# Optimization experiments

Measured on AMD Instinct MI355X. Metric: run time of the kernel, lower is better.

## Reference

```python
import jax, jax.numpy as jnp
import numpy as np

DVEC = 128
B, S = 4, 1024


def setup_inputs() -> dict:
    key = jax.random.key(0)
    k1, k2 = jax.random.split(key)
    func_and_arg = jax.random.normal(k1, (B, S, 2 * DVEC), dtype=jnp.float32)
    cooccurrences = jax.random.normal(k2, (DVEC, DVEC, DVEC), dtype=jnp.float32)
    return {"func_and_arg": func_and_arg, "cooccurrences": cooccurrences}


def reference(func_and_arg, cooccurrences):
    # out[b,s,z] = sum_{i,j} func[b,s,i] * cooc[i,j,z] * arg[b,s,j]
    d = cooccurrences.shape[0]
    func = func_and_arg[..., :d]   # [B,S,D]
    arg = func_and_arg[..., d:]    # [B,S,D]
    # contract func over i first -> [B,S,D(j),Z], then arg over j -> [B,S,Z]
    tmp = jnp.einsum('bsi,ijz->bsjz', func, cooccurrences)
    return jnp.einsum('bsjz,bsj->bsz', tmp, arg)
```

## Files before the change

### kernel.cpp

```cpp
#include <hip/hip_runtime.h>
#include <hip/hip_bf16.h>


typedef __attribute__((ext_vector_type(8))) short bf16x8;
typedef __attribute__((ext_vector_type(4))) float f32x4;

__device__ __forceinline__ unsigned pkbf16(float x, float y) {
    __hip_bfloat162 h = __float22bfloat162_rn(make_float2(x, y));
    unsigned u; __builtin_memcpy(&u, &h, sizeof(u));
    return u;
}

template<int USE_WS>
__global__ __launch_bounds__(256, 2) void cooc_main(
    const float* __restrict__ fa, const float* __restrict__ Cc,
    float* __restrict__ dst)
{
    __shared__ __align__(16) ushort bT[2][64 * 136];
    __shared__ float f_lds[16][128];

    const int bid   = blockIdx.x;
    const int kp    = bid & 7;
    const int zp    = (bid >> 3) & 1;
    const int mtile = bid >> 4;
    const int t0 = mtile * 128;
    const int i0 = kp * 16;
    const int z0 = zp * 64;

    const int tid  = threadIdx.x;
    const int lane = tid & 63;
    const int wv = tid >> 6;
    const int mg = wv >> 1;
    const int zg = wv & 1;
    const int lm = lane & 15;
    const int lk = lane >> 4;

    {
        const int row = tid & 127;
        const int sh = (tid >> 7) * 8;
        const float* fp = fa + (size_t)(t0 + row) * 256 + i0 + sh;
        float4 v0 = *(const float4*)fp;
        float4 v1 = *(const float4*)(fp + 4);
        f_lds[sh + 0][row] = v0.x; f_lds[sh + 1][row] = v0.y;
        f_lds[sh + 2][row] = v0.z; f_lds[sh + 3][row] = v0.w;
        f_lds[sh + 4][row] = v1.x; f_lds[sh + 5][row] = v1.y;
        f_lds[sh + 6][row] = v1.z; f_lds[sh + 7][row] = v1.w;
    }

    union { unsigned u[4]; bf16x8 v; } a_pk[4][4];
    #pragma unroll
    for (int m = 0; m < 4; ++m) {
        const float* ab = fa + (size_t)(t0 + mg * 64 + m * 16 + lm) * 256 + 128;
        #pragma unroll
        for (int ks = 0; ks < 4; ++ks) {
            float4 q0 = *(const float4*)(ab + ks * 32 + lk * 8);
            float4 q1 = *(const float4*)(ab + ks * 32 + lk * 8 + 4);
            a_pk[m][ks].u[0] = pkbf16(q0.x, q0.y);
            a_pk[m][ks].u[1] = pkbf16(q0.z, q0.w);
            a_pk[m][ks].u[2] = pkbf16(q1.x, q1.y);
            a_pk[m][ks].u[3] = pkbf16(q1.z, q1.w);
        }
    }

    const int zq  = tid & 15;
    const int jq0 = tid >> 4;
    const float* csrc0 = Cc + (size_t)i0 * 16384 + (size_t)(jq0 * 4) * 128 + z0 + zq * 4;
    const float* csrc1 = csrc0 + 16 * 4 * 128;
    union { float4 v4[4]; float f[16]; } La[2];

    auto loads = [&](int s) {
        const float* p0 = csrc0 + (size_t)s * 16384;
        const float* p1 = csrc1 + (size_t)s * 16384;
        #pragma unroll
        for (int r = 0; r < 4; ++r) {
            La[0].v4[r] = *(const float4*)(p0 + r * 128);
            La[1].v4[r] = *(const float4*)(p1 + r * 128);
        }
    };
    auto writes = [&](int b) {
        #pragma unroll
        for (int part = 0; part < 2; ++part) {
            const int jq = jq0 + part * 16;
            const int pos = ((jq >> 1) + zq) & 15;
            #pragma unroll
            for (int rr = 0; rr < 4; ++rr) {
                const int zl = zq * 4 + rr;
                const unsigned lo = pkbf16(La[part].f[0 * 4 + rr], La[part].f[1 * 4 + rr]);
                const unsigned hi = pkbf16(La[part].f[2 * 4 + rr], La[part].f[3 * 4 + rr]);
                *(uint2*)&bT[b][zl * 136 + pos * 8 + (jq & 1) * 4] = make_uint2(lo, hi);
            }
        }
    };

    loads(0); writes(0);
    __syncthreads();

    float acc[4][2][4];
    #pragma unroll
    for (int m = 0; m < 4; ++m)
        #pragma unroll
        for (int n = 0; n < 2; ++n)
            #pragma unroll
            for (int r = 0; r < 4; ++r) acc[m][n][r] = 0.f;

    #pragma unroll 2
    for (int s = 0; s < 16; ++s) {
        const int p = s & 1;
        if (s < 15) loads(s + 1);

        float4 f4[4];
        #pragma unroll
        for (int m = 0; m < 4; ++m)
            f4[m] = *(const float4*)&f_lds[s][mg * 64 + m * 16 + lk * 4];

        bf16x8 Bf[4][2];
        #pragma unroll
        for (int ks = 0; ks < 4; ++ks)
            #pragma unroll
            for (int n = 0; n < 2; ++n) {
                const int zz = zg * 32 + n * 16 + lm;
                const int pos = ((ks * 4 + lk) + (zz >> 2)) & 15;
                Bf[ks][n] = *(const bf16x8*)&bT[p][zz * 136 + pos * 8];
            }

        #pragma unroll
        for (int m = 0; m < 4; ++m)
            #pragma unroll
            for (int n = 0; n < 2; ++n) {
                f32x4 g = {0.f, 0.f, 0.f, 0.f};
                #pragma unroll
                for (int ks = 0; ks < 4; ++ks)
                    g = __builtin_amdgcn_mfma_f32_16x16x32_bf16(a_pk[m][ks].v, Bf[ks][n], g, 0, 0, 0);
                acc[m][n][0] += f4[m].x * g[0];
                acc[m][n][1] += f4[m].y * g[1];
                acc[m][n][2] += f4[m].z * g[2];
                acc[m][n][3] += f4[m].w * g[3];
            }

        if (s < 15) writes(p ^ 1);
        __syncthreads();
    }

    #pragma unroll
    for (int m = 0; m < 4; ++m)
        #pragma unroll
        for (int n = 0; n < 2; ++n)
            #pragma unroll
            for (int r = 0; r < 4; ++r) {
                const int row = t0 + mg * 64 + m * 16 + lk * 4 + r;
                const int col = z0 + zg * 32 + n * 16 + lm;
                if (USE_WS)
                    dst[(size_t)kp * 524288 + (size_t)row * 128 + col] = acc[m][n][r];
                else
                    atomicAdd(&dst[(size_t)row * 128 + col], acc[m][n][r]);
            }
}

__global__ __launch_bounds__(256) void cooc_reduce(const float* __restrict__ ws,
                                                   float* __restrict__ out) {
    const size_t idx = ((size_t)blockIdx.x * 256 + threadIdx.x) * 4;
    float4 a = *(const float4*)(ws + idx);
    #pragma unroll
    for (int k = 1; k < 8; ++k) {
        float4 b = *(const float4*)(ws + (size_t)k * 524288 + idx);
        a.x += b.x; a.y += b.y; a.z += b.z; a.w += b.w;
    }
    *(float4*)(out + idx) = a;
}

extern "C" void kernel_launch(void* const* d_in, const int* in_sizes, int n_in,
                              void* d_out, int out_size, void* d_ws, size_t ws_size,
                              hipStream_t stream) {
    const float* fa = (const float*)d_in[0];
    const float* Cc = (const float*)d_in[1];
    float* out = (float*)d_out;

    const bool use_ws = ws_size >= (size_t)8 * 524288 * sizeof(float);
    if (use_ws) {
        cooc_main<1><<<512, 256, 0, stream>>>(fa, Cc, (float*)d_ws);
        cooc_reduce<<<512, 256, 0, stream>>>((const float*)d_ws, out);
    } else {
        (void)hipMemsetAsync(out, 0, (size_t)out_size * sizeof(float), stream);
        cooc_main<0><<<512, 256, 0, stream>>>(fa, Cc, out);
    }
}
```

Baseline: 92.06 us.

## Pre-transpose cooccurrence tensor to bf16 and load MFMA B operands from global

Adds a pre-pass kernel that converts the cooccurrence tensor to bf16 in a z-major transposed layout in workspace. The main kernel then reads B fragments straight from global memory into registers, double-buffered, with no LDS staging or per-step barriers. Each wave now covers all 128 rows for a 16-column slice, holding 8 A tiles in registers. This removes the per-block fp32 conversion, the LDS transpose and the synchronisation, in exchange for an extra launch, extra workspace traffic and higher register pressure. The old path is kept as a fallback for small workspaces.

Result: slower. 104.5 us (+13.6%).

```diff
diff --git a/kernel.cpp b/kernel.cpp
--- a/kernel.cpp
+++ b/kernel.cpp
@@ -11,29 +11,48 @@
     return u;
 }
 
+__global__ __launch_bounds__(256) void cooc_transpose(
+    const float* __restrict__ Cc, ushort* __restrict__ CT)
+{
+    __shared__ float tile[32][132];
+    const int i  = blockIdx.x >> 2;
+    const int j0 = (blockIdx.x & 3) * 32;
+    const int t  = threadIdx.x;
+
+    {
+        const int jj = t >> 3;
+        const int zb = (t & 7) * 16;
+        const float* src = Cc + (size_t)i * 16384 + (size_t)(j0 + jj) * 128 + zb;
+        #pragma unroll
+        for (int k = 0; k < 4; ++k)
+            *(float4*)&tile[jj][zb + k * 4] = *(const float4*)(src + k * 4);
+    }
+    __syncthreads();
+    {
+        const int z = t >> 1;
+        const int h = t & 1;
+        unsigned o[8];
+        #pragma unroll
+        for (int p = 0; p < 8; ++p)
+            o[p] = pkbf16(tile[h * 16 + 2 * p][z], tile[h * 16 + 2 * p + 1][z]);
+        ushort* dst = CT + (size_t)i * 16384 + (size_t)z * 128 + j0 + h * 16;
+        *(uint4*)dst       = make_uint4(o[0], o[1], o[2], o[3]);
+        *(uint4*)(dst + 8) = make_uint4(o[4], o[5], o[6], o[7]);
+    }
+}
+
 template<int USE_WS>
 __global__ __launch_bounds__(256, 2) void cooc_main(
-    const float* __restrict__ fa, const float* __restrict__ Cc,
+    const float* __restrict__ fa, const ushort* __restrict__ CT,
     float* __restrict__ dst)
 {
-    __shared__ __align__(16) ushort bT[2][64 * 136];
     __shared__ float f_lds[16][128];
 
-    const int bid   = blockIdx.x;
-    const int kp    = bid & 7;
-    const int zp    = (bid >> 3) & 1;
-    const int mtile = bid >> 4;
-    const int t0 = mtile * 128;
-    const int i0 = kp * 16;
-    const int z0 = zp * 64;
-
-    const int tid  = threadIdx.x;
-    const int lane = tid & 63;
-    const int wv = tid >> 6;
-    const int mg = wv >> 1;
-    const int zg = wv & 1;
-    const int lm = lane & 15;
-    const int lk = lane >> 4;
+    const int bid = blockIdx.x;
+    const int kp = bid & 7, zp = (bid >> 3) & 1, mtile = bid >> 4;
+    const int t0 = mtile * 128, i0 = kp * 16, z0 = zp * 64;
+    const int tid = threadIdx.x, lane = tid & 63, wv = tid >> 6;
+    const int lm = lane & 15, lk = lane >> 4;
 
     {
         const int row = tid & 127;
@@ -47,10 +66,10 @@
         f_lds[sh + 6][row] = v1.z; f_lds[sh + 7][row] = v1.w;
     }
 
-    union { unsigned u[4]; bf16x8 v; } a_pk[4][4];
-    #pragma unroll
-    for (int m = 0; m < 4; ++m) {
-        const float* ab = fa + (size_t)(t0 + mg * 64 + m * 16 + lm) * 256 + 128;
+    union { unsigned u[4]; bf16x8 v; } a_pk[8][4];
+    #pragma unroll
+    for (int m = 0; m < 8; ++m) {
+        const float* ab = fa + (size_t)(t0 + m * 16 + lm) * 256 + 128;
         #pragma unroll
         for (int ks = 0; ks < 4; ++ks) {
             float4 q0 = *(const float4*)(ab + ks * 32 + lk * 8);
@@ -61,13 +80,110 @@
             a_pk[m][ks].u[3] = pkbf16(q1.z, q1.w);
         }
     }
-
-    const int zq  = tid & 15;
-    const int jq0 = tid >> 4;
+    __syncthreads();
+
+    const ushort* bsrc = CT + (size_t)i0 * 16384
+                            + (size_t)(z0 + wv * 16 + lm) * 128 + lk * 8;
+
+    bf16x8 B[2][4];
+    #pragma unroll
+    for (int ks = 0; ks < 4; ++ks)
+        B[0][ks] = *(const bf16x8*)(bsrc + ks * 32);
+
+    float acc[8][4];
+    #pragma unroll
+    for (int m = 0; m < 8; ++m)
+        #pragma unroll
+        for (int r = 0; r < 4; ++r) acc[m][r] = 0.f;
+
+    #pragma unroll 2
+    for (int s = 0; s < 16; ++s) {
+        const int cur = s & 1;
+        if (s < 15) {
+            const ushort* p = bsrc + (size_t)(s + 1) * 16384;
+            #pragma unroll
+            for (int ks = 0; ks < 4; ++ks)
+                B[cur ^ 1][ks] = *(const bf16x8*)(p + ks * 32);
+        }
+        #pragma unroll
+        for (int m = 0; m < 8; ++m) {
+            float4 f4 = *(const float4*)&f_lds[s][m * 16 + lk * 4];
+            f32x4 g = {0.f, 0.f, 0.f, 0.f};
+            #pragma unroll
+            for (int ks = 0; ks < 4; ++ks)
+                g = __builtin_amdgcn_mfma_f32_16x16x32_bf16(a_pk[m][ks].v, B[cur][ks], g, 0, 0, 0);
+            acc[m][0] += f4.x * g[0];
+            acc[m][1] += f4.y * g[1];
+            acc[m][2] += f4.z * g[2];
+            acc[m][3] += f4.w * g[3];
+        }
+    }
+
+    const int col = z0 + wv * 16 + lm;
+    #pragma unroll
+    for (int m = 0; m < 8; ++m)
+        #pragma unroll
+        for (int r = 0; r < 4; ++r) {
+            const int row = t0 + m * 16 + lk * 4 + r;
+            if (USE_WS)
+                dst[(size_t)kp * 524288 + (size_t)row * 128 + col] = acc[m][r];
+            else
+                atomicAdd(&dst[(size_t)row * 128 + col], acc[m][r]);
+        }
+}
+
+__global__ __launch_bounds__(256) void cooc_reduce(const float* __restrict__ ws,
+                                                   float* __restrict__ out) {
+    const size_t idx = ((size_t)blockIdx.x * 256 + threadIdx.x) * 4;
+    float4 a = *(const float4*)(ws + idx);
+    #pragma unroll
+    for (int k = 1; k < 8; ++k) {
+        float4 b = *(const float4*)(ws + (size_t)k * 524288 + idx);
+        a.x += b.x; a.y += b.y; a.z += b.z; a.w += b.w;
+    }
+    *(float4*)(out + idx) = a;
+}
+
+__global__ __launch_bounds__(256, 2) void cooc_fb(
+    const float* __restrict__ fa, const float* __restrict__ Cc,
+    float* __restrict__ dst)
+{
+    __shared__ __align__(16) ushort bT[2][64 * 136];
+    __shared__ float f_lds[16][128];
+    const int bid = blockIdx.x;
+    const int kp = bid & 7, zp = (bid >> 3) & 1, mtile = bid >> 4;
+    const int t0 = mtile * 128, i0 = kp * 16, z0 = zp * 64;
+    const int tid = threadIdx.x, lane = tid & 63, wv = tid >> 6;
+    const int mg = wv >> 1, zg = wv & 1, lm = lane & 15, lk = lane >> 4;
+    {
+        const int row = tid & 127;
+        const int sh = (tid >> 7) * 8;
+        const float* fp = fa + (size_t)(t0 + row) * 256 + i0 + sh;
+        float4 v0 = *(const float4*)fp;
+        float4 v1 = *(const float4*)(fp + 4);
+        f_lds[sh + 0][row] = v0.x; f_lds[sh + 1][row] = v0.y;
+        f_lds[sh + 2][row] = v0.z; f_lds[sh + 3][row] = v0.w;
+        f_lds[sh + 4][row] = v1.x; f_lds[sh + 5][row] = v1.y;
+        f_lds[sh + 6][row] = v1.z; f_lds[sh + 7][row] = v1.w;
+    }
+    union { unsigned u[4]; bf16x8 v; } a_pk[4][4];
+    #pragma unroll
+    for (int m = 0; m < 4; ++m) {
+        const float* ab = fa + (size_t)(t0 + mg * 64 + m * 16 + lm) * 256 + 128;
+        #pragma unroll
+        for (int ks = 0; ks < 4; ++ks) {
+            float4 q0 = *(const float4*)(ab + ks * 32 + lk * 8);
+            float4 q1 = *(const float4*)(ab + ks * 32 + lk * 8 + 4);
+            a_pk[m][ks].u[0] = pkbf16(q0.x, q0.y);
+            a_pk[m][ks].u[1] = pkbf16(q0.z, q0.w);
+            a_pk[m][ks].u[2] = pkbf16(q1.x, q1.y);
+            a_pk[m][ks].u[3] = pkbf16(q1.z, q1.w);
+        }
+    }
+    const int zq = tid & 15, jq0 = tid >> 4;
     const float* csrc0 = Cc + (size_t)i0 * 16384 + (size_t)(jq0 * 4) * 128 + z0 + zq * 4;
     const float* csrc1 = csrc0 + 16 * 4 * 128;
     union { float4 v4[4]; float f[16]; } La[2];
-
     auto loads = [&](int s) {
         const float* p0 = csrc0 + (size_t)s * 16384;
         const float* p1 = csrc1 + (size_t)s * 16384;
@@ -91,10 +207,8 @@
             }
         }
     };
-
     loads(0); writes(0);
     __syncthreads();
-
     float acc[4][2][4];
     #pragma unroll
     for (int m = 0; m < 4; ++m)
@@ -102,17 +216,14 @@
         for (int n = 0; n < 2; ++n)
             #pragma unroll
             for (int r = 0; r < 4; ++r) acc[m][n][r] = 0.f;
-
     #pragma unroll 2
     for (int s = 0; s < 16; ++s) {
         const int p = s & 1;
         if (s < 15) loads(s + 1);
-
         float4 f4[4];
         #pragma unroll
         for (int m = 0; m < 4; ++m)
             f4[m] = *(const float4*)&f_lds[s][mg * 64 + m * 16 + lk * 4];
-
         bf16x8 Bf[4][2];
         #pragma unroll
         for (int ks = 0; ks < 4; ++ks)
@@ -122,7 +233,6 @@
                 const int pos = ((ks * 4 + lk) + (zz >> 2)) & 15;
                 Bf[ks][n] = *(const bf16x8*)&bT[p][zz * 136 + pos * 8];
             }
-
         #pragma unroll
         for (int m = 0; m < 4; ++m)
             #pragma unroll
@@ -136,11 +246,9 @@
                 acc[m][n][2] += f4[m].z * g[2];
                 acc[m][n][3] += f4[m].w * g[3];
             }
-
         if (s < 15) writes(p ^ 1);
         __syncthreads();
     }
-
     #pragma unroll
     for (int m = 0; m < 4; ++m)
         #pragma unroll
@@ -149,23 +257,8 @@
             for (int r = 0; r < 4; ++r) {
                 const int row = t0 + mg * 64 + m * 16 + lk * 4 + r;
                 const int col = z0 + zg * 32 + n * 16 + lm;
-                if (USE_WS)
-                    dst[(size_t)kp * 524288 + (size_t)row * 128 + col] = acc[m][n][r];
-                else
-                    atomicAdd(&dst[(size_t)row * 128 + col], acc[m][n][r]);
-            }
-}
-
-__global__ __launch_bounds__(256) void cooc_reduce(const float* __restrict__ ws,
-                                                   float* __restrict__ out) {
-    const size_t idx = ((size_t)blockIdx.x * 256 + threadIdx.x) * 4;
-    float4 a = *(const float4*)(ws + idx);
-    #pragma unroll
-    for (int k = 1; k < 8; ++k) {
-        float4 b = *(const float4*)(ws + (size_t)k * 524288 + idx);
-        a.x += b.x; a.y += b.y; a.z += b.z; a.w += b.w;
-    }
-    *(float4*)(out + idx) = a;
+                atomicAdd(&dst[(size_t)row * 128 + col], acc[m][n][r]);
+            }
 }
 
 extern "C" void kernel_launch(void* const* d_in, const int* in_sizes, int n_in,
@@ -175,12 +268,23 @@
     const float* Cc = (const float*)d_in[1];
     float* out = (float*)d_out;
 
-    const bool use_ws = ws_size >= (size_t)8 * 524288 * sizeof(float);
-    if (use_ws) {
-        cooc_main<1><<<512, 256, 0, stream>>>(fa, Cc, (float*)d_ws);
+    const size_t PART = (size_t)8 * 524288;
+    const size_t CTOF = PART * sizeof(float);
+    const size_t NEED_FULL = CTOF + (size_t)128 * 128 * 128 * 2;
+    const size_t NEED_CT   = (size_t)128 * 128 * 128 * 2;
+
+    if (ws_size >= NEED_FULL) {
+        ushort* CT = (ushort*)((char*)d_ws + CTOF);
+        cooc_transpose<<<512, 256, 0, stream>>>(Cc, CT);
+        cooc_main<1><<<512, 256, 0, stream>>>(fa, CT, (float*)d_ws);
         cooc_reduce<<<512, 256, 0, stream>>>((const float*)d_ws, out);
+    } else if (ws_size >= NEED_CT) {
+        ushort* CT = (ushort*)d_ws;
+        cooc_transpose<<<512, 256, 0, stream>>>(Cc, CT);
+        (void)hipMemsetAsync(out, 0, (size_t)out_size * sizeof(float), stream);
+        cooc_main<0><<<512, 256, 0, stream>>>(fa, CT, out);
     } else {
         (void)hipMemsetAsync(out, 0, (size_t)out_size * sizeof(float), stream);
-        cooc_main<0><<<512, 256, 0, stream>>>(fa, Cc, out);
-    }
-}
+        cooc_fb<<<512, 256, 0, stream>>>(fa, Cc, out);
+    }
+}
```
